# Kernel optimization log

Hardware: AMD Instinct MI355X
Metric: run time of the kernel (lower is better)

Reference implementation:

```python
import jax, jax.numpy as jnp
import numpy as np

# Geometry from the hard-coded `options` tensor
VIEWS, DETS = 160, 640
H, W = 416, 416
D_IMG = 0.006641            # image pixel size
D_DET = 0.012858            # detector bin size
ANG0 = 0.0
D_ANG = 0.009817477 * 4     # = 2*pi/160 (full scan)
S2R = 5.95                  # source-to-rotation-center distance
D2R = 4.906                 # detector-to-rotation-center distance
VIRDET = D_DET * S2R / (S2R + D2R)   # detector rescaled to isocenter (virtual detector)
PI = float(np.pi)
COEF = PI / VIEWS
BATCH = 32


def setup_inputs() -> dict:
    key = jax.random.key(0)
    projection = jax.random.normal(key, (BATCH, 1, VIEWS, DETS), dtype=jnp.float32)

    # Ramp filter (Ram-Lak, spatial domain), length 2*dets-1, exactly as in torch __init__
    x = np.arange(2 * DETS - 1) - DETS + 1
    x_safe = np.where(x == 0, 1, x).astype(np.float64)
    filt = np.where(np.abs(x) % 2 == 1,
                    -1.0 / (PI * PI * x_safe * x_safe * VIRDET * VIRDET),
                    0.0)
    filt[x == 0] = 1.0 / (4.0 * VIRDET * VIRDET)
    filt = jnp.asarray(filt.reshape(1, 1, 1, -1), dtype=jnp.float32)

    # Cosine (fan-beam) pre-weighting, detector bin centers at (i - dets/2 + 0.5)*virdet
    u = (np.arange(DETS) - DETS / 2 + 0.5) * VIRDET
    wv = S2R / np.sqrt(S2R ** 2 + u ** 2) * VIRDET
    w = jnp.asarray(wv.reshape(1, 1, 1, -1), dtype=jnp.float32)

    return {"projection": projection, "w": w, "filt": filt}


def _backproject(p):
    """Pixel-driven equidistant fan-beam backprojection.
    p: filtered sinogram [B, 1, VIEWS, DETS] -> recon [B, 1, H, W].
    """
    betas = ANG0 + D_ANG * jnp.arange(VIEWS, dtype=jnp.float32)
    xs = (jnp.arange(W, dtype=jnp.float32) - (W - 1) / 2.0) * D_IMG   # [W]
    ys = ((H - 1) / 2.0 - jnp.arange(H, dtype=jnp.float32)) * D_IMG   # [H]
    Xg, Yg = jnp.meshgrid(xs, ys)   # both [H, W]

    pv = jnp.moveaxis(p, 2, 0)  # [VIEWS, B, 1, DETS]

    def step(acc, inp):
        beta, pb = inp                      # pb: [B, 1, DETS]
        cb, sb = jnp.cos(beta), jnp.sin(beta)
        d = Xg * cb + Yg * sb               # pixel component toward source
        r = -Xg * sb + Yg * cb              # perpendicular component
        U = S2R - d                         # source-to-pixel depth
        # detector coordinate at isocenter -> fractional bin index
        idx = (S2R * r / U) / VIRDET + (DETS - 1) / 2.0   # [H, W]
        valid = (idx >= 0.0) & (idx <= DETS - 1)
        i0 = jnp.clip(jnp.floor(idx), 0, DETS - 2).astype(jnp.int32)
        frac = jnp.clip(idx - i0.astype(jnp.float32), 0.0, 1.0)
        # irregular gather + linear interpolation: [B,1,H,W]
        v = pb[:, :, i0] * (1.0 - frac) + pb[:, :, i0 + 1] * frac
        wgt = jnp.where(valid, (S2R / U) ** 2, 0.0)       # distance weighting
        return acc + wgt * v, None

    init = jnp.zeros((p.shape[0], 1, H, W), dtype=p.dtype)
    acc, _ = jax.lax.scan(step, init, (betas, pv))
    return acc


def reference(projection, w, filt):
    # 1) cosine weighting (elementwise broadcast over detector axis)
    p = projection * w
    p = jax.lax.conv_general_dilated(
        p, filt, window_strides=(1, 1),
        padding=((0, 0), (DETS - 1, DETS - 1)),
        dimension_numbers=("NCHW", "OIHW", "NCHW"))
    # 3) geometric backprojection + angular step normalization
    return COEF * _backproject(p)
```

## Files before the change

kernel.cpp:

```cpp
#include <hip/hip_runtime.h>

#define VIEWS 160
#define DETS  640
#define H_IMG 416
#define W_IMG 416
#define BATCH 32

constexpr double D_IMG_D  = 0.006641;
constexpr double D_DET_D  = 0.012858;
constexpr double S2R_D    = 5.95;
constexpr double D2R_D    = 4.906;
constexpr double VIRDET_D = D_DET_D * S2R_D / (S2R_D + D2R_D);
constexpr double PI_D     = 3.14159265358979323846;

typedef __fp16 __attribute__((ext_vector_type(2))) h2f;

#define TILES_X 13
#define TILES_Y 52
#define NTILES  (TILES_X * TILES_Y)
#define NB      64

__global__ __launch_bounds__(160) void prep_kernel(float* __restrict__ vcs,
                                                   int* __restrict__ bs_tab) {
    int v    = threadIdx.x;
    int tile = blockIdx.x;
    float dang = (float)(0.009817477 * 4.0);
    float beta = dang * (float)v;
    float cb = cosf(beta), sb = sinf(beta);
    float K  = (float)(S2R_D / VIRDET_D);
    if (tile == 0) {
        ((float4*)vcs)[v] = make_float4(cb, sb, -K * sb, K * cb);
    }
    int ty = tile / TILES_X, tx = tile - ty * TILES_X;
    float XL = ((float)(tx * 32) - 207.5f) * (float)D_IMG_D;
    float XR = ((float)(tx * 32 + 31) - 207.5f) * (float)D_IMG_D;
    float YT = (207.5f - (float)(ty * 8)) * (float)D_IMG_D;
    float YB = (207.5f - (float)(ty * 8 + 7)) * (float)D_IMG_D;
    float m = 1e30f;
#define CORNER(Xc, Yc) { \
        float r_ = -(Xc) * sb + (Yc) * cb; \
        float U_ = (float)S2R_D - (Xc) * cb - (Yc) * sb; \
        float ix = fmaf(K, r_ / U_, 319.5f); \
        m = fminf(m, ix); }
    CORNER(XL, YT); CORNER(XR, YT); CORNER(XL, YB); CORNER(XR, YB);
#undef CORNER
    int bs = (int)floorf(m) - 2;
    bs = max(0, min(DETS - NB, bs)) & ~1;
    bs_tab[tile * VIEWS + v] = bs;
}

#define FT 320
#define RPAD 24
#define RSTR 209
__global__ __launch_bounds__(FT) void filter_kernel(
    const float* __restrict__ proj, const float* __restrict__ w,
    const float* __restrict__ filt, unsigned int* __restrict__ pf) {
    __shared__ float4 s_in[4 * RSTR];
    __shared__ float  s_f[2 * DETS];
    __shared__ unsigned int s_out[2 * DETS];

    int t = threadIdx.x;
    int g = blockIdx.x;
    int group4 = g / 160;
    int v = g - group4 * 160;

    for (int e = t; e < 4 * RSTR; e += FT) {
        int ri = e / RSTR, c4 = e - ri * RSTR;
        float4 pv = make_float4(0.f, 0.f, 0.f, 0.f);
        if (c4 >= RPAD && c4 < RPAD + 160) {
            int b = group4 * 4 + ri;
            pv = ((const float4*)(proj + ((size_t)b * VIEWS + v) * DETS))[c4 - RPAD];
            float4 wv = ((const float4*)w)[c4 - RPAD];
            pv.x *= wv.x; pv.y *= wv.y; pv.z *= wv.z; pv.w *= wv.w;
        }
        s_in[e] = pv;
    }
    for (int e = t; e < 2 * DETS; e += FT) s_f[e] = (e < 2 * DETS - 1) ? filt[e] : 0.f;
    __syncthreads();

    int sub = (t >= 160) ? 1 : 0;
    int tj  = t - sub * 160;

    const float4* f4  = (const float4*)s_f;
    const float4* in4 = &s_in[sub * 2 * RSTR + tj];
    float4 o0 = {0,0,0,0}, o1 = {0,0,0,0};
    float4 fp = f4[135];
    #pragma unroll 2
    for (int u = 0; u < 50; ++u) {
        float4 fn = f4[136 + u];
        {
            float4 iv = in4[0 * RSTR + u];
            o0.x = fmaf(iv.x, fp.w, o0.x); o0.x = fmaf(iv.y, fn.x, o0.x);
            o0.x = fmaf(iv.z, fn.y, o0.x); o0.x = fmaf(iv.w, fn.z, o0.x);
            o0.y = fmaf(iv.x, fp.z, o0.y); o0.y = fmaf(iv.y, fp.w, o0.y);
            o0.y = fmaf(iv.z, fn.x, o0.y); o0.y = fmaf(iv.w, fn.y, o0.y);
            o0.z = fmaf(iv.x, fp.y, o0.z); o0.z = fmaf(iv.y, fp.z, o0.z);
            o0.z = fmaf(iv.z, fp.w, o0.z); o0.z = fmaf(iv.w, fn.x, o0.z);
            o0.w = fmaf(iv.x, fp.x, o0.w); o0.w = fmaf(iv.y, fp.y, o0.w);
            o0.w = fmaf(iv.z, fp.z, o0.w); o0.w = fmaf(iv.w, fp.w, o0.w);
        }
        {
            float4 iv = in4[1 * RSTR + u];
            o1.x = fmaf(iv.x, fp.w, o1.x); o1.x = fmaf(iv.y, fn.x, o1.x);
            o1.x = fmaf(iv.z, fn.y, o1.x); o1.x = fmaf(iv.w, fn.z, o1.x);
            o1.y = fmaf(iv.x, fp.z, o1.y); o1.y = fmaf(iv.y, fp.w, o1.y);
            o1.y = fmaf(iv.z, fn.x, o1.y); o1.y = fmaf(iv.w, fn.y, o1.y);
            o1.z = fmaf(iv.x, fp.y, o1.z); o1.z = fmaf(iv.y, fp.z, o1.z);
            o1.z = fmaf(iv.z, fp.w, o1.z); o1.z = fmaf(iv.w, fn.x, o1.z);
            o1.w = fmaf(iv.x, fp.x, o1.w); o1.w = fmaf(iv.y, fp.y, o1.w);
            o1.w = fmaf(iv.z, fp.z, o1.w); o1.w = fmaf(iv.w, fp.w, o1.w);
        }
        fp = fn;
    }

    float coef = (float)((PI_D / (double)VIEWS) * S2R_D * S2R_D);
    auto h0 = __builtin_amdgcn_cvt_pkrtz(o0.x * coef, o1.x * coef);
    auto h1 = __builtin_amdgcn_cvt_pkrtz(o0.y * coef, o1.y * coef);
    auto h2 = __builtin_amdgcn_cvt_pkrtz(o0.z * coef, o1.z * coef);
    auto h3 = __builtin_amdgcn_cvt_pkrtz(o0.w * coef, o1.w * coef);
    uint4 pk = make_uint4(__builtin_bit_cast(unsigned int, h0),
                          __builtin_bit_cast(unsigned int, h1),
                          __builtin_bit_cast(unsigned int, h2),
                          __builtin_bit_cast(unsigned int, h3));
    *(uint4*)&s_out[sub * DETS + 4 * tj] = pk;
    __syncthreads();

    unsigned int a0 = s_out[2 * t],        a1 = s_out[2 * t + 1];
    unsigned int b0 = s_out[DETS + 2 * t], b1 = s_out[DETS + 2 * t + 1];
    uint4 o = make_uint4(a0, b0, a1, b1);
    ((uint4*)(pf + ((size_t)v * 8 + group4) * (2 * DETS)))[t] = o;
}

__device__ __forceinline__ void gld_lds16(const char* g, char* l) {
    __builtin_amdgcn_global_load_lds(
        (const __attribute__((address_space(1))) unsigned int*)g,
        (__attribute__((address_space(3))) unsigned int*)l, 16, 0, 0);
}

__global__ __launch_bounds__(256, 8) void bp_kernel(
    const unsigned int* __restrict__ pf, const float* __restrict__ vcs,
    const int* __restrict__ bs_tab, float* __restrict__ out) {
    __shared__ alignas(16) unsigned int s_buf[4 * 1024];

    int t    = threadIdx.x;
    int half = blockIdx.z;
    int tile = blockIdx.y * TILES_X + blockIdx.x;
    int x    = blockIdx.x * 32 + (t & 31);
    int y    = blockIdx.y * 8 + (t >> 5);

    float X  = ((float)x - 207.5f) * (float)D_IMG_D;
    float Yv = (207.5f - (float)y) * (float)D_IMG_D;

    int vbase = half * (VIEWS / 2);
    const float4* vc4 = (const float4*)vcs + vbase;
    const int*    bsp = bs_tab + tile * VIEWS + vbase;
    const char*   pfb = (const char*)pf + (size_t)vbase * 40960;
    int  goff  = (t >> 5) * (DETS * 8) + (t & 31) * 16;
    int  ldoff = (t >> 6) << 10;

    float acc[32];
    #pragma unroll
    for (int b = 0; b < 32; ++b) acc[b] = 0.f;
    h2f hacc[16];
    #pragma unroll
    for (int p = 0; p < 16; ++p) hacc[p] = (h2f)0.f;

    #pragma unroll
    for (int d = 0; d < 3; ++d) {
        int bsd = bsp[d];
        gld_lds16(pfb + (size_t)d * 40960 + (size_t)bsd * 8 + goff,
                  (char*)s_buf + (d << 12) + ldoff);
    }

    for (int c = 0; c < VIEWS / 2; ++c) {
        asm volatile("s_waitcnt vmcnt(2)" ::: "memory");
        __builtin_amdgcn_s_barrier();
        __builtin_amdgcn_sched_barrier(0);

        {
            int vn  = min(c + 3, VIEWS / 2 - 1);
            int bsn = bsp[vn];
            gld_lds16(pfb + (size_t)vn * 40960 + (size_t)bsn * 8 + goff,
                      (char*)s_buf + (((c + 3) & 3) << 12) + ldoff);
        }

        float4 a  = vc4[c];
        int    bsc = bsp[c];
        float U   = fmaf(-X, a.x, fmaf(-Yv, a.y, (float)S2R_D));
        float num = fmaf(X, a.z, Yv * a.w);
        float ru   = __builtin_amdgcn_rcpf(U);
        float idx  = fmaf(num, ru, 319.5f);
        float idxc = __builtin_amdgcn_fmed3f(idx, 0.f, 639.f);
        float i0f  = fminf(idxc, 638.0f);
        int   i0   = (int)i0f;
        float frac = idxc - truncf(i0f);
        float w2   = ru * ru;
        float wgt  = (idx == idxc) ? w2 : 0.f;
        float w1f  = wgt * frac;
        float w0f  = wgt - w1f;
        h2f w0h = __builtin_amdgcn_cvt_pkrtz(w0f, w0f);
        h2f w1h = __builtin_amdgcn_cvt_pkrtz(w1f, w1f);
        int bl = min(max(i0 - bsc, 0), NB - 2);
        const uint2* L = (const uint2*)((const char*)s_buf + ((c & 3) << 12)) + bl;
        #pragma unroll
        for (int gg = 0; gg < 8; ++gg) {
            uint2 A = L[gg * NB];
            uint2 B = L[gg * NB + 1];
            h2f pa = __builtin_bit_cast(h2f, A.x);
            h2f pb = __builtin_bit_cast(h2f, B.x);
            h2f pc = __builtin_bit_cast(h2f, A.y);
            h2f pd = __builtin_bit_cast(h2f, B.y);
            hacc[2 * gg]     = __builtin_elementwise_fma(pa, w0h, hacc[2 * gg]);
            hacc[2 * gg]     = __builtin_elementwise_fma(pb, w1h, hacc[2 * gg]);
            hacc[2 * gg + 1] = __builtin_elementwise_fma(pc, w0h, hacc[2 * gg + 1]);
            hacc[2 * gg + 1] = __builtin_elementwise_fma(pd, w1h, hacc[2 * gg + 1]);
        }
        if ((c & 7) == 7) {
            #pragma unroll
            for (int gg = 0; gg < 8; ++gg) {
                acc[4 * gg + 0] += (float)hacc[2 * gg].x;
                acc[4 * gg + 1] += (float)hacc[2 * gg].y;
                acc[4 * gg + 2] += (float)hacc[2 * gg + 1].x;
                acc[4 * gg + 3] += (float)hacc[2 * gg + 1].y;
                hacc[2 * gg] = (h2f)0.f; hacc[2 * gg + 1] = (h2f)0.f;
            }
        }
    }

    float* ob = out + (size_t)y * W_IMG + x;
    #pragma unroll
    for (int b = 0; b < 32; ++b)
        unsafeAtomicAdd(ob + (size_t)b * (H_IMG * W_IMG), acc[b]);
}

extern "C" void kernel_launch(void* const* d_in, const int* in_sizes, int n_in,
                              void* d_out, int out_size, void* d_ws, size_t ws_size,
                              hipStream_t stream) {
    const float* proj = (const float*)d_in[0];
    const float* w    = (const float*)d_in[1];
    const float* filt = (const float*)d_in[2];
    float* out = (float*)d_out;

    float*        vcs    = (float*)d_ws;
    int*          bs_tab = (int*)((char*)d_ws + 4096);
    unsigned int* pf     = (unsigned int*)((char*)d_ws + 4096 + 432640);

    hipMemsetAsync(d_out, 0, (size_t)BATCH * H_IMG * W_IMG * sizeof(float), stream);
    prep_kernel<<<NTILES, 160, 0, stream>>>(vcs, bs_tab);
    filter_kernel<<<(BATCH / 4) * VIEWS, FT, 0, stream>>>(proj, w, filt, pf);
    bp_kernel<<<dim3(TILES_X, TILES_Y, 2), 256, 0, stream>>>(pf, vcs, bs_tab, out);
}
```

Measured before the change: 197.2 us.

## Split backprojection views three ways, double-buffer LDS, fold output zeroing into init

The backprojection grid now splits the 160 views into three z-chunks instead of two, giving more blocks to fill the GPU at the cost of one more atomic-add pass per output pixel. The LDS staging drops from a 4-deep prefetch ring with explicit vmcnt waits to a 2-buffer scheme with __syncthreads. That halves shared memory but makes latency hiding shallower. The separate hipMemsetAsync is removed: the precompute kernel (now 256 threads) zeroes the output with float4 stores, saving one launch. A final fp16-to-fp32 accumulator flush is added because chunk lengths are no longer multiples of 8.

```diff
diff --git a/kernel.cpp b/kernel.cpp
--- a/kernel.cpp
+++ b/kernel.cpp
@@ -19,34 +19,43 @@
 #define TILES_Y 52
 #define NTILES  (TILES_X * TILES_Y)
 #define NB      64
-
-__global__ __launch_bounds__(160) void prep_kernel(float* __restrict__ vcs,
-                                                   int* __restrict__ bs_tab) {
-    int v    = threadIdx.x;
+#define ZSPLIT  3
+
+__global__ __launch_bounds__(256) void init_kernel(float* __restrict__ vcs,
+                                                   int* __restrict__ bs_tab,
+                                                   float4* __restrict__ out4) {
+    int t    = threadIdx.x;
     int tile = blockIdx.x;
-    float dang = (float)(0.009817477 * 4.0);
-    float beta = dang * (float)v;
-    float cb = cosf(beta), sb = sinf(beta);
-    float K  = (float)(S2R_D / VIRDET_D);
-    if (tile == 0) {
-        ((float4*)vcs)[v] = make_float4(cb, sb, -K * sb, K * cb);
-    }
-    int ty = tile / TILES_X, tx = tile - ty * TILES_X;
-    float XL = ((float)(tx * 32) - 207.5f) * (float)D_IMG_D;
-    float XR = ((float)(tx * 32 + 31) - 207.5f) * (float)D_IMG_D;
-    float YT = (207.5f - (float)(ty * 8)) * (float)D_IMG_D;
-    float YB = (207.5f - (float)(ty * 8 + 7)) * (float)D_IMG_D;
-    float m = 1e30f;
+    if (t < VIEWS) {
+        int v = t;
+        float dang = (float)(0.009817477 * 4.0);
+        float beta = dang * (float)v;
+        float cb = cosf(beta), sb = sinf(beta);
+        float K  = (float)(S2R_D / VIRDET_D);
+        if (tile == 0) {
+            ((float4*)vcs)[v] = make_float4(cb, sb, -K * sb, K * cb);
+        }
+        int ty = tile / TILES_X, tx = tile - ty * TILES_X;
+        float XL = ((float)(tx * 32) - 207.5f) * (float)D_IMG_D;
+        float XR = ((float)(tx * 32 + 31) - 207.5f) * (float)D_IMG_D;
+        float YT = (207.5f - (float)(ty * 8)) * (float)D_IMG_D;
+        float YB = (207.5f - (float)(ty * 8 + 7)) * (float)D_IMG_D;
+        float m = 1e30f;
 #define CORNER(Xc, Yc) { \
         float r_ = -(Xc) * sb + (Yc) * cb; \
         float U_ = (float)S2R_D - (Xc) * cb - (Yc) * sb; \
         float ix = fmaf(K, r_ / U_, 319.5f); \
         m = fminf(m, ix); }
-    CORNER(XL, YT); CORNER(XR, YT); CORNER(XL, YB); CORNER(XR, YB);
+        CORNER(XL, YT); CORNER(XR, YT); CORNER(XL, YB); CORNER(XR, YB);
 #undef CORNER
-    int bs = (int)floorf(m) - 2;
-    bs = max(0, min(DETS - NB, bs)) & ~1;
-    bs_tab[tile * VIEWS + v] = bs;
+        int bs = (int)floorf(m) - 2;
+        bs = max(0, min(DETS - NB, bs)) & ~1;
+        bs_tab[tile * VIEWS + v] = bs;
+    }
+    size_t base = (size_t)tile * 2048 + t;
+    float4 z = make_float4(0.f, 0.f, 0.f, 0.f);
+    #pragma unroll
+    for (int i = 0; i < 8; ++i) out4[base + (size_t)i * 256] = z;
 }
 
 #define FT 320
@@ -140,10 +149,10 @@
 __global__ __launch_bounds__(256, 8) void bp_kernel(
     const unsigned int* __restrict__ pf, const float* __restrict__ vcs,
     const int* __restrict__ bs_tab, float* __restrict__ out) {
-    __shared__ alignas(16) unsigned int s_buf[4 * 1024];
+    __shared__ alignas(16) unsigned int s_buf[2 * 1024];
 
     int t    = threadIdx.x;
-    int half = blockIdx.z;
+    int zc   = blockIdx.z;
     int tile = blockIdx.y * TILES_X + blockIdx.x;
     int x    = blockIdx.x * 32 + (t & 31);
     int y    = blockIdx.y * 8 + (t >> 5);
@@ -151,10 +160,12 @@
     float X  = ((float)x - 207.5f) * (float)D_IMG_D;
     float Yv = (207.5f - (float)y) * (float)D_IMG_D;
 
-    int vbase = half * (VIEWS / 2);
-    const float4* vc4 = (const float4*)vcs + vbase;
-    const int*    bsp = bs_tab + tile * VIEWS + vbase;
-    const char*   pfb = (const char*)pf + (size_t)vbase * 40960;
+    int vstart = (zc * VIEWS) / ZSPLIT;
+    int vend   = ((zc + 1) * VIEWS) / ZSPLIT;
+    int nv     = vend - vstart;
+    const float4* vc4 = (const float4*)vcs + vstart;
+    const int*    bsp = bs_tab + tile * VIEWS + vstart;
+    const char*   pfb = (const char*)pf + (size_t)vstart * 40960;
     int  goff  = (t >> 5) * (DETS * 8) + (t & 31) * 16;
     int  ldoff = (t >> 6) << 10;
 
@@ -165,24 +176,17 @@
     #pragma unroll
     for (int p = 0; p < 16; ++p) hacc[p] = (h2f)0.f;
 
-    #pragma unroll
-    for (int d = 0; d < 3; ++d) {
-        int bsd = bsp[d];
-        gld_lds16(pfb + (size_t)d * 40960 + (size_t)bsd * 8 + goff,
-                  (char*)s_buf + (d << 12) + ldoff);
-    }
-
-    for (int c = 0; c < VIEWS / 2; ++c) {
-        asm volatile("s_waitcnt vmcnt(2)" ::: "memory");
-        __builtin_amdgcn_s_barrier();
-        __builtin_amdgcn_sched_barrier(0);
-
-        {
-            int vn  = min(c + 3, VIEWS / 2 - 1);
-            int bsn = bsp[vn];
-            gld_lds16(pfb + (size_t)vn * 40960 + (size_t)bsn * 8 + goff,
-                      (char*)s_buf + (((c + 3) & 3) << 12) + ldoff);
-        }
+    #define STAGE(c) do { \
+        int bsd = bsp[(c)]; \
+        gld_lds16(pfb + (size_t)(c) * 40960 + (size_t)bsd * 8 + goff, \
+                  (char*)s_buf + (((c) & 1) << 12) + ldoff); \
+    } while (0)
+
+    STAGE(0);
+    __syncthreads();
+
+    for (int c = 0; c < nv; ++c) {
+        if (c + 1 < nv) STAGE(c + 1);
 
         float4 a  = vc4[c];
         int    bsc = bsp[c];
@@ -201,7 +205,7 @@
         h2f w0h = __builtin_amdgcn_cvt_pkrtz(w0f, w0f);
         h2f w1h = __builtin_amdgcn_cvt_pkrtz(w1f, w1f);
         int bl = min(max(i0 - bsc, 0), NB - 2);
-        const uint2* L = (const uint2*)((const char*)s_buf + ((c & 3) << 12)) + bl;
+        const uint2* L = (const uint2*)((const char*)s_buf + ((c & 1) << 12)) + bl;
         #pragma unroll
         for (int gg = 0; gg < 8; ++gg) {
             uint2 A = L[gg * NB];
@@ -225,6 +229,16 @@
                 hacc[2 * gg] = (h2f)0.f; hacc[2 * gg + 1] = (h2f)0.f;
             }
         }
+        __syncthreads();
+    }
+    #undef STAGE
+
+    #pragma unroll
+    for (int gg = 0; gg < 8; ++gg) {
+        acc[4 * gg + 0] += (float)hacc[2 * gg].x;
+        acc[4 * gg + 1] += (float)hacc[2 * gg].y;
+        acc[4 * gg + 2] += (float)hacc[2 * gg + 1].x;
+        acc[4 * gg + 3] += (float)hacc[2 * gg + 1].y;
     }
 
     float* ob = out + (size_t)y * W_IMG + x;
@@ -245,8 +259,7 @@
     int*          bs_tab = (int*)((char*)d_ws + 4096);
     unsigned int* pf     = (unsigned int*)((char*)d_ws + 4096 + 432640);
 
-    hipMemsetAsync(d_out, 0, (size_t)BATCH * H_IMG * W_IMG * sizeof(float), stream);
-    prep_kernel<<<NTILES, 160, 0, stream>>>(vcs, bs_tab);
+    init_kernel<<<NTILES, 256, 0, stream>>>(vcs, bs_tab, (float4*)out);
     filter_kernel<<<(BATCH / 4) * VIEWS, FT, 0, stream>>>(proj, w, filt, pf);
-    bp_kernel<<<dim3(TILES_X, TILES_Y, 2), 256, 0, stream>>>(pf, vcs, bs_tab, out);
-}
+    bp_kernel<<<dim3(TILES_X, TILES_Y, ZSPLIT), 256, 0, stream>>>(pf, vcs, bs_tab, out);
+}
```

Result: faster. 190.7 us (-3.3%).
